# Optimization experiments

Measured on AMD Instinct MI355X. Metric: run time of the kernel, lower is better.

Reference implementation:

```python
import jax, jax.numpy as jnp
import numpy as np

N_GRAPHS = 64

def setup_inputs() -> dict:
    key = jax.random.key(0)
    ks = jax.random.split(key, 8)
    N, E, H = 50000, 600000, 128
    x = jax.random.normal(ks[0], (N, 2), dtype=jnp.float32)
    edge_index = jax.random.randint(ks[1], (2, E), 0, N, dtype=jnp.int64)
    batch = jnp.sort(jax.random.randint(ks[2], (N,), 0, N_GRAPHS, dtype=jnp.int64))
    s = 0.1  # keep tanh out of saturation
    return {
        'x': x,
        'edge_index': edge_index,
        'batch': batch,
        'W1': jax.random.normal(ks[3], (2, H), dtype=jnp.float32) * s,
        'b1': jnp.zeros((H,), jnp.float32),
        'W2': jax.random.normal(ks[4], (H, H), dtype=jnp.float32) * s,
        'b2': jnp.zeros((H,), jnp.float32),
        'W3': jax.random.normal(ks[5], (H, H), dtype=jnp.float32) * s,
        'b3': jnp.zeros((H,), jnp.float32),
        'Wo': jax.random.normal(ks[6], (2 * H, 41), dtype=jnp.float32) * s,
        'bo': jnp.zeros((41,), jnp.float32),
    }

def reference(x, edge_index, batch, W1, b1, W2, b2, W3, b3, Wo, bo):
    N = x.shape[0]
    src, dst = edge_index[0], edge_index[1]
    # GCN symmetric normalization with self loops: deg = in-degree + 1
    ones_e = jnp.ones(src.shape[0], dtype=x.dtype)
    deg = jax.ops.segment_sum(ones_e, dst, num_segments=N) + 1.0
    dinv = jax.lax.rsqrt(deg)                       # [N]
    edge_norm = (dinv[src] * dinv[dst])[:, None]    # [E,1]
    self_norm = (dinv * dinv)[:, None]              # [N,1]

    def gcn(h, W, b):
        h = h @ W                                   # [N,H] transform first
        agg = jax.ops.segment_sum(h[src] * edge_norm, dst, num_segments=N)
        return agg + h * self_norm + b

    h = jnp.tanh(gcn(x, W1, b1))
    h = jnp.tanh(gcn(h, W2, b2))
    h = jnp.tanh(gcn(h, W3, b3))

    # global max pool + global mean pool over graphs
    cnt = jax.ops.segment_sum(jnp.ones(N, dtype=h.dtype), batch, num_segments=N_GRAPHS)
    mx = jax.ops.segment_max(h, batch, num_segments=N_GRAPHS)
    mx = jnp.where(cnt[:, None] > 0, mx, 0.0)
    mean = jax.ops.segment_sum(h, batch, num_segments=N_GRAPHS) / jnp.maximum(cnt, 1.0)[:, None]
    pooled = jnp.concatenate([mx, mean], axis=1)    # [G, 2H]
    return jnp.tanh(pooled @ Wo + bo)               # [G, 41]
```

## Files before the change

### kernel.cpp

```cpp
#include <hip/hip_runtime.h>
#include <math.h>

#define NGRAPH 64
#define SCAN_BLK 1024
#define COLCAP 6144

typedef short short8 __attribute__((ext_vector_type(8)));
typedef float floatx4 __attribute__((ext_vector_type(4)));

__device__ inline unsigned pack_bf16x2(float a, float b) {
    unsigned ua = __float_as_uint(a);
    unsigned ub = __float_as_uint(b);
    ua = (ua + 0x7fffu + ((ua >> 16) & 1u)) >> 16;
    ub = (ub + 0x7fffu + ((ub >> 16) & 1u)) >> 16;
    return ua | (ub << 16);
}
__device__ inline unsigned short bf16_1(float a) {
    unsigned ua = __float_as_uint(a);
    return (unsigned short)((ua + 0x7fffu + ((ua >> 16) & 1u)) >> 16);
}
__device__ inline float bf16lo(unsigned u) { return __uint_as_float(u << 16); }
__device__ inline float bf16hi(unsigned u) { return __uint_as_float(u & 0xffff0000u); }

__device__ inline unsigned fkey(float v) {
    unsigned u = __float_as_uint(v);
    return (v >= 0.f) ? (u | 0x80000000u) : ~u;
}


#define TIDX(u) ((size_t)((qb + (unsigned)(u)) * 4u + (unsigned)q))
#define ACC4() do {                                                       \
    uint4 v0 = t4[TIDX(u0)]; uint4 v1 = t4[TIDX(u1)];                     \
    uint4 v2 = t4[TIDX(u2)]; uint4 v3 = t4[TIDX(u3)];                     \
    a[0] += bf16lo(v0.x); a[1] += bf16hi(v0.x);                           \
    a[2] += bf16lo(v0.y); a[3] += bf16hi(v0.y);                           \
    a[4] += bf16lo(v0.z); a[5] += bf16hi(v0.z);                           \
    a[6] += bf16lo(v0.w); a[7] += bf16hi(v0.w);                           \
    a[0] += bf16lo(v1.x); a[1] += bf16hi(v1.x);                           \
    a[2] += bf16lo(v1.y); a[3] += bf16hi(v1.y);                           \
    a[4] += bf16lo(v1.z); a[5] += bf16hi(v1.z);                           \
    a[6] += bf16lo(v1.w); a[7] += bf16hi(v1.w);                           \
    a[0] += bf16lo(v2.x); a[1] += bf16hi(v2.x);                           \
    a[2] += bf16lo(v2.y); a[3] += bf16hi(v2.y);                           \
    a[4] += bf16lo(v2.z); a[5] += bf16hi(v2.z);                           \
    a[6] += bf16lo(v2.w); a[7] += bf16hi(v2.w);                           \
    a[0] += bf16lo(v3.x); a[1] += bf16hi(v3.x);                           \
    a[2] += bf16lo(v3.y); a[3] += bf16hi(v3.y);                           \
    a[4] += bf16lo(v3.z); a[5] += bf16hi(v3.z);                           \
    a[6] += bf16lo(v3.w); a[7] += bf16hi(v3.w);                           \
} while (0)
#define ACC4M() do {                                                      \
    uint4 v0 = t4[TIDX(u0)]; uint4 v1 = t4[TIDX(u1)];                     \
    uint4 v2 = t4[TIDX(u2)]; uint4 v3 = t4[TIDX(u3)];                     \
    a[0] += bf16lo(v0.x); a[1] += bf16hi(v0.x);                           \
    a[2] += bf16lo(v0.y); a[3] += bf16hi(v0.y);                           \
    a[4] += bf16lo(v0.z); a[5] += bf16hi(v0.z);                           \
    a[6] += bf16lo(v0.w); a[7] += bf16hi(v0.w);                           \
    a[0] = fmaf(m1, bf16lo(v1.x), a[0]); a[1] = fmaf(m1, bf16hi(v1.x), a[1]); \
    a[2] = fmaf(m1, bf16lo(v1.y), a[2]); a[3] = fmaf(m1, bf16hi(v1.y), a[3]); \
    a[4] = fmaf(m1, bf16lo(v1.z), a[4]); a[5] = fmaf(m1, bf16hi(v1.z), a[5]); \
    a[6] = fmaf(m1, bf16lo(v1.w), a[6]); a[7] = fmaf(m1, bf16hi(v1.w), a[7]); \
    a[0] = fmaf(m2, bf16lo(v2.x), a[0]); a[1] = fmaf(m2, bf16hi(v2.x), a[1]); \
    a[2] = fmaf(m2, bf16lo(v2.y), a[2]); a[3] = fmaf(m2, bf16hi(v2.y), a[3]); \
    a[4] = fmaf(m2, bf16lo(v2.z), a[4]); a[5] = fmaf(m2, bf16hi(v2.z), a[5]); \
    a[6] = fmaf(m2, bf16lo(v2.w), a[6]); a[7] = fmaf(m2, bf16hi(v2.w), a[7]); \
    a[0] = fmaf(m3, bf16lo(v3.x), a[0]); a[1] = fmaf(m3, bf16hi(v3.x), a[1]); \
    a[2] = fmaf(m3, bf16lo(v3.y), a[2]); a[3] = fmaf(m3, bf16hi(v3.y), a[3]); \
    a[4] = fmaf(m3, bf16lo(v3.z), a[4]); a[5] = fmaf(m3, bf16hi(v3.z), a[5]); \
    a[6] = fmaf(m3, bf16lo(v3.w), a[6]); a[7] = fmaf(m3, bf16hi(v3.w), a[7]); \
} while (0)


__global__ void pack_count(const int* __restrict__ dst, int E, int* __restrict__ cnt,
                           const float* __restrict__ W2, const float* __restrict__ W3,
                           unsigned* __restrict__ Wt2, unsigned* __restrict__ Wt3) {
    if (blockIdx.x < 32) {
        int b = blockIdx.x;
        const float* W = (b < 16) ? W2 : W3;
        unsigned* Wt = (b < 16) ? Wt2 : Wt3;
        b &= 15;
        int bk = b & 3, bn = b >> 2;
        __shared__ float s[32][33];
        int tx = threadIdx.x & 31, ty = threadIdx.x >> 5;
#pragma unroll
        for (int r = 0; r < 4; ++r)
            s[r * 8 + ty][tx] = W[(bk * 32 + r * 8 + ty) * 128 + bn * 32 + tx];
        __syncthreads();
        int t16 = threadIdx.x & 15, tn = threadIdx.x >> 4;
#pragma unroll
        for (int pass = 0; pass < 2; ++pass) {
            int nl = pass * 16 + tn;
            unsigned pk = pack_bf16x2(s[2 * t16][nl], s[2 * t16 + 1][nl]);
            Wt[(bn * 32 + nl) * 64 + bk * 16 + t16] = pk;
        }
    } else {
        int e = (blockIdx.x - 32) * blockDim.x + threadIdx.x;
        if (e < E) atomicAdd(&cnt[dst[e]], 1);
    }
}


__global__ __launch_bounds__(SCAN_BLK) void scanA(const int* __restrict__ cnt,
                                                  const float* __restrict__ x,
                                                  int* __restrict__ row_ptr,
                                                  int* __restrict__ bsum,
                                                  float* __restrict__ dinv,
                                                  float2* __restrict__ y,
                                                  const int* __restrict__ batch,
                                                  int* __restrict__ ticket,
                                                  int* __restrict__ goff, int N) {
    __shared__ int sm[SCAN_BLK];
    __shared__ int amLast;
    int i = blockIdx.x * SCAN_BLK + threadIdx.x;
    int v = (i < N) ? cnt[i] : 0;
    if (i < N) {
        float dv = rsqrtf((float)v + 1.0f);
        dinv[i] = dv;
        float2 xv = ((const float2*)x)[i];
        y[i] = make_float2(xv.x * dv, xv.y * dv);
    }
    sm[threadIdx.x] = v;
    __syncthreads();
    for (int off = 1; off < SCAN_BLK; off <<= 1) {
        int t = (threadIdx.x >= (unsigned)off) ? sm[threadIdx.x - off] : 0;
        __syncthreads();
        sm[threadIdx.x] += t;
        __syncthreads();
    }
    if (i < N) row_ptr[i] = sm[threadIdx.x] - v;
    if (threadIdx.x == SCAN_BLK - 1) bsum[blockIdx.x] = sm[SCAN_BLK - 1];
    __syncthreads();
    if (threadIdx.x == 0) {
        __threadfence();
        amLast = (atomicAdd(ticket, 1) == (int)gridDim.x - 1);
    }
    __syncthreads();
    if (!amLast) return;
    int nb = (int)gridDim.x;
    int v2 = (threadIdx.x < (unsigned)nb) ? atomicAdd(&bsum[threadIdx.x], 0) : 0;
    sm[threadIdx.x] = v2;
    __syncthreads();
    for (int off = 1; off < SCAN_BLK; off <<= 1) {
        int t = (threadIdx.x >= (unsigned)off) ? sm[threadIdx.x - off] : 0;
        __syncthreads();
        sm[threadIdx.x] += t;
        __syncthreads();
    }
    if (threadIdx.x < (unsigned)nb) bsum[threadIdx.x] = sm[threadIdx.x] - v2;
    if (threadIdx.x <= NGRAPH) {
        int g = threadIdx.x;
        int lo = 0, hi = N;
        while (lo < hi) {
            int mid = (lo + hi) >> 1;
            if (batch[mid] < g) lo = mid + 1; else hi = mid;
        }
        goff[g] = lo;
    }
}

__global__ void fill_kernel(const int* __restrict__ src, const int* __restrict__ dst, int E,
                            const int* __restrict__ row_ptr, const int* __restrict__ bsum,
                            int* __restrict__ cnt, int* __restrict__ col) {
    int e = blockIdx.x * blockDim.x + threadIdx.x;
    if (e < E) {
        int d = dst[e];
        int base = row_ptr[d] + bsum[d >> 10];
        int p = base + atomicSub(&cnt[d], 1) - 1;
        col[p] = src[e];
    }
}


__global__ __launch_bounds__(256) void agg_x_t1(const float2* __restrict__ y,
                                                const int* __restrict__ row_ptr,
                                                const int* __restrict__ bsum,
                                                const int* __restrict__ col,
                                                const float* __restrict__ dinv,
                                                const float* __restrict__ W1,
                                                const float* __restrict__ b1,
                                                unsigned short* __restrict__ h, int N, int E) {
    __shared__ float4 sW[64];
    __shared__ float4 sb[32];
    __shared__ float2 zs[256];
    if (threadIdx.x < 64) sW[threadIdx.x] = ((const float4*)W1)[threadIdx.x];
    if (threadIdx.x < 32) sb[threadIdx.x] = ((const float4*)b1)[threadIdx.x];

    int v = blockIdx.x * 256 + threadIdx.x;
    float2 zv = make_float2(0.f, 0.f);
    if (v < N) {
        int s = row_ptr[v] + bsum[v >> 10];
        int e = (v + 1 < N) ? row_ptr[v + 1] + bsum[(v + 1) >> 10] : E;
        float2 a0 = y[v];
        float2 a1 = make_float2(0.f, 0.f);
        float2 a2 = make_float2(0.f, 0.f);
        float2 a3 = make_float2(0.f, 0.f);
        int j = s;
        for (; j + 4 <= e; j += 4) {
            int u0 = col[j], u1 = col[j + 1], u2 = col[j + 2], u3 = col[j + 3];
            float2 v0 = y[u0], v1 = y[u1], v2 = y[u2], v3 = y[u3];
            a0.x += v0.x; a0.y += v0.y;
            a1.x += v1.x; a1.y += v1.y;
            a2.x += v2.x; a2.y += v2.y;
            a3.x += v3.x; a3.y += v3.y;
        }
        for (; j < e; ++j) {
            float2 vv = y[col[j]];
            a0.x += vv.x; a0.y += vv.y;
        }
        float dv = dinv[v];
        zv = make_float2(dv * (a0.x + a1.x + a2.x + a3.x),
                         dv * (a0.y + a1.y + a2.y + a3.y));
    }
    zs[threadIdx.x] = zv;
    __syncthreads();

    int q = threadIdx.x & 31;
    int rsub = threadIdx.x >> 5;
    float4 w0 = sW[q];
    float4 w1 = sW[32 + q];
    float4 b = sb[q];
    size_t qoff = (size_t)(q >> 3) * N;
#pragma unroll 4
    for (int pass = 0; pass < 32; ++pass) {
        int local = pass * 8 + rsub;
        int row = blockIdx.x * 256 + local;
        if (row >= N) break;
        float2 z = zs[local];
        float ox = tanhf(fmaf(z.x, w0.x, fmaf(z.y, w1.x, b.x)));
        float oy = tanhf(fmaf(z.x, w0.y, fmaf(z.y, w1.y, b.y)));
        float oz = tanhf(fmaf(z.x, w0.z, fmaf(z.y, w1.z, b.z)));
        float ow = tanhf(fmaf(z.x, w0.w, fmaf(z.y, w1.w, b.w)));
        uint2 pk;
        pk.x = pack_bf16x2(ox, oy);
        pk.y = pack_bf16x2(oz, ow);
        ((uint2*)h)[(qoff + row) * 8 + (q & 7)] = pk;
    }
}


__global__ __launch_bounds__(256) void gemm_mfma(const unsigned short* __restrict__ A,
                                                 const unsigned* __restrict__ Wt,
                                                 const float* __restrict__ dinv,
                                                 unsigned short* __restrict__ t, int N) {
    __shared__ unsigned sW[128 * 68];
    const uint4* Wt4 = (const uint4*)Wt;
    for (int i = threadIdx.x; i < 2048; i += 256) {
        int n = i >> 4, c = i & 15;
        *(uint4*)&sW[n * 68 + c * 4] = Wt4[i];
    }
    __syncthreads();
    int l = threadIdx.x & 63;
    int w = threadIdx.x >> 6;
    int lm = l & 15;
    int q4 = l >> 4;

    floatx4 acc[2][8];
#pragma unroll
    for (int i = 0; i < 2; ++i)
#pragma unroll
        for (int j = 0; j < 8; ++j) acc[i][j] = (floatx4){0.f, 0.f, 0.f, 0.f};

    int rowbase = blockIdx.x * 128 + w * 32;
    int k8 = q4 * 8;
#pragma unroll
    for (int ks = 0; ks < 4; ++ks) {
        short8 a[2];
#pragma unroll
        for (int mt = 0; mt < 2; ++mt) {
            int r = min(rowbase + mt * 16 + lm, N - 1);
            a[mt] = *(const short8*)(A + ((size_t)ks * N + r) * 32 + k8);
        }
#pragma unroll
        for (int nt = 0; nt < 8; ++nt) {
            short8 b = *(const short8*)&sW[(nt * 16 + lm) * 68 + ks * 16 + q4 * 4];
#pragma unroll
            for (int mt = 0; mt < 2; ++mt)
                acc[mt][nt] = __builtin_amdgcn_mfma_f32_16x16x32_bf16(b, a[mt], acc[mt][nt], 0, 0, 0);
        }
    }

#pragma unroll
    for (int mt = 0; mt < 2; ++mt) {
        int gr = rowbase + mt * 16 + lm;
        if (gr < N) {
            float dv = dinv[gr];
#pragma unroll
            for (int nt = 0; nt < 8; ++nt) {
                uint2 pk;
                pk.x = pack_bf16x2(acc[mt][nt][0] * dv, acc[mt][nt][1] * dv);
                pk.y = pack_bf16x2(acc[mt][nt][2] * dv, acc[mt][nt][3] * dv);
                *(uint2*)(t + ((size_t)(nt >> 1) * N + gr) * 32 + (nt & 1) * 16 + q4 * 4) = pk;
            }
        }
    }
}


__global__ __launch_bounds__(1024) void agg_kernel(const unsigned short* __restrict__ t,
                                                   const int* __restrict__ row_ptr,
                                                   const int* __restrict__ bsum,
                                                   const int* __restrict__ col,
                                                   const float* __restrict__ dinv,
                                                   const float* __restrict__ bias,
                                                   unsigned short* __restrict__ out, int N, int E) {
    int nchunk = (N + 255) >> 8;
    int bid = (int)blockIdx.x;
    int r8 = bid & 7;
    int qt = r8 >> 1;
    int c = (bid >> 3) * 2 + (r8 & 1);
    if (c >= nchunk) return;

    __shared__ int scol[COLCAP];
    int firstNode = c * 256;
    int lastNode = min(firstNode + 256, N);
    int sBase = row_ptr[firstNode] + bsum[firstNode >> 10];
    int eEnd = (lastNode < N) ? row_ptr[lastNode] + bsum[lastNode >> 10] : E;
    int range = eEnd - sBase;
    bool inLds = (range <= COLCAP);
    if (inLds) {
        for (int i = threadIdx.x; i < range; i += 1024) scol[i] = col[sBase + i];
    }
    __syncthreads();

    int q = threadIdx.x & 3;
    int node = firstNode + ((int)threadIdx.x >> 2);
    if (node >= N) return;
    const uint4* t4 = (const uint4*)t;
    unsigned qb = (unsigned)qt * (unsigned)N;
    int s = row_ptr[node] + bsum[node >> 10];
    int e = (node + 1 < N) ? row_ptr[node + 1] + bsum[(node + 1) >> 10] : E;
    int deg = e - s;

    float a[8];
    {
        uint4 v = t4[TIDX(node)];
        a[0] = bf16lo(v.x); a[1] = bf16hi(v.x);
        a[2] = bf16lo(v.y); a[3] = bf16hi(v.y);
        a[4] = bf16lo(v.z); a[5] = bf16hi(v.z);
        a[6] = bf16lo(v.w); a[7] = bf16hi(v.w);
    }
    int j = 0;
    if (inLds) {
        int sl = s - sBase;
        for (; j + 4 <= deg; j += 4) {
            int u0 = scol[sl + j], u1 = scol[sl + j + 1];
            int u2 = scol[sl + j + 2], u3 = scol[sl + j + 3];
            ACC4();
        }
        if (j < deg) {
            float m1 = (j + 1 < deg) ? 1.f : 0.f;
            float m2 = (j + 2 < deg) ? 1.f : 0.f;
            float m3 = (j + 3 < deg) ? 1.f : 0.f;
            int u0 = scol[sl + j];
            int u1 = scol[sl + min(j + 1, deg - 1)];
            int u2 = scol[sl + min(j + 2, deg - 1)];
            int u3 = scol[sl + min(j + 3, deg - 1)];
            ACC4M();
        }
    } else {
        for (; j + 4 <= deg; j += 4) {
            int u0 = col[s + j], u1 = col[s + j + 1];
            int u2 = col[s + j + 2], u3 = col[s + j + 3];
            ACC4();
        }
        if (j < deg) {
            float m1 = (j + 1 < deg) ? 1.f : 0.f;
            float m2 = (j + 2 < deg) ? 1.f : 0.f;
            float m3 = (j + 3 < deg) ? 1.f : 0.f;
            int u0 = col[s + j];
            int u1 = col[s + min(j + 1, deg - 1)];
            int u2 = col[s + min(j + 2, deg - 1)];
            int u3 = col[s + min(j + 3, deg - 1)];
            ACC4M();
        }
    }

    float dv = dinv[node];
    const float4* b4 = (const float4*)bias;
    float4 b0 = b4[qt * 8 + q * 2];
    float4 b1 = b4[qt * 8 + q * 2 + 1];
    uint4 pk;
    pk.x = pack_bf16x2(tanhf(fmaf(dv, a[0], b0.x)), tanhf(fmaf(dv, a[1], b0.y)));
    pk.y = pack_bf16x2(tanhf(fmaf(dv, a[2], b0.z)), tanhf(fmaf(dv, a[3], b0.w)));
    pk.z = pack_bf16x2(tanhf(fmaf(dv, a[4], b1.x)), tanhf(fmaf(dv, a[5], b1.y)));
    pk.w = pack_bf16x2(tanhf(fmaf(dv, a[6], b1.z)), tanhf(fmaf(dv, a[7], b1.w)));
    ((uint4*)out)[TIDX(node)] = pk;
}


__global__ __launch_bounds__(1024) void agg3_pool(const unsigned short* __restrict__ t,
                                                  const int* __restrict__ row_ptr,
                                                  const int* __restrict__ bsum,
                                                  const int* __restrict__ col,
                                                  const float* __restrict__ dinv,
                                                  const float* __restrict__ bias,
                                                  const int* __restrict__ batch,
                                                  unsigned* __restrict__ pmax,
                                                  float* __restrict__ psum, int N, int E) {
    int nchunk = (N + 255) >> 8;
    int bid = (int)blockIdx.x;
    int r8 = bid & 7;
    int qt = r8 >> 1;
    int c = (bid >> 3) * 2 + (r8 & 1);
    if (c >= nchunk) return;

    __shared__ unsigned smax[2][32];
    __shared__ float ssum[2][32];
    __shared__ int scol[COLCAP];
    if (threadIdx.x < 64) {
        smax[threadIdx.x >> 5][threadIdx.x & 31] = 0u;
        ssum[threadIdx.x >> 5][threadIdx.x & 31] = 0.f;
    }
    int firstNode = c * 256;
    int lastNode = min(firstNode + 256, N);
    int sBase = row_ptr[firstNode] + bsum[firstNode >> 10];
    int eEnd = (lastNode < N) ? row_ptr[lastNode] + bsum[lastNode >> 10] : E;
    int range = eEnd - sBase;
    bool inLds = (range <= COLCAP);
    if (inLds) {
        for (int i = threadIdx.x; i < range; i += 1024) scol[i] = col[sBase + i];
    }
    __syncthreads();

    int q = threadIdx.x & 3;
    int blockBase = firstNode;
    int node = blockBase + ((int)threadIdx.x >> 2);
    bool valid = node < N;
    int nc = valid ? node : N - 1;
    const uint4* t4 = (const uint4*)t;
    unsigned qb = (unsigned)qt * (unsigned)N;
    int s = row_ptr[nc] + bsum[nc >> 10];
    int e = (nc + 1 < N) ? row_ptr[nc + 1] + bsum[(nc + 1) >> 10] : E;
    int deg = valid ? (e - s) : 0;

    float a[8];
    {
        uint4 v = t4[TIDX(nc)];
        a[0] = bf16lo(v.x); a[1] = bf16hi(v.x);
        a[2] = bf16lo(v.y); a[3] = bf16hi(v.y);
        a[4] = bf16lo(v.z); a[5] = bf16hi(v.z);
        a[6] = bf16lo(v.w); a[7] = bf16hi(v.w);
    }
    int j = 0;
    if (inLds) {
        int sl = s - sBase;
        for (; j + 4 <= deg; j += 4) {
            int u0 = scol[sl + j], u1 = scol[sl + j + 1];
            int u2 = scol[sl + j + 2], u3 = scol[sl + j + 3];
            ACC4();
        }
        if (j < deg) {
            float m1 = (j + 1 < deg) ? 1.f : 0.f;
            float m2 = (j + 2 < deg) ? 1.f : 0.f;
            float m3 = (j + 3 < deg) ? 1.f : 0.f;
            int u0 = scol[sl + j];
            int u1 = scol[sl + min(j + 1, deg - 1)];
            int u2 = scol[sl + min(j + 2, deg - 1)];
            int u3 = scol[sl + min(j + 3, deg - 1)];
            ACC4M();
        }
    } else {
        for (; j + 4 <= deg; j += 4) {
            int u0 = col[s + j], u1 = col[s + j + 1];
            int u2 = col[s + j + 2], u3 = col[s + j + 3];
            ACC4();
        }
        if (j < deg) {
            float m1 = (j + 1 < deg) ? 1.f : 0.f;
            float m2 = (j + 2 < deg) ? 1.f : 0.f;
            float m3 = (j + 3 < deg) ? 1.f : 0.f;
            int u0 = col[s + j];
            int u1 = col[s + min(j + 1, deg - 1)];
            int u2 = col[s + min(j + 2, deg - 1)];
            int u3 = col[s + min(j + 3, deg - 1)];
            ACC4M();
        }
    }

    float dv = dinv[nc];
    const float4* b4 = (const float4*)bias;
    float4 b0 = b4[qt * 8 + q * 2];
    float4 b1 = b4[qt * 8 + q * 2 + 1];
    float o[8];
    o[0] = tanhf(fmaf(dv, a[0], b0.x)); o[1] = tanhf(fmaf(dv, a[1], b0.y));
    o[2] = tanhf(fmaf(dv, a[2], b0.z)); o[3] = tanhf(fmaf(dv, a[3], b0.w));
    o[4] = tanhf(fmaf(dv, a[4], b1.x)); o[5] = tanhf(fmaf(dv, a[5], b1.y));
    o[6] = tanhf(fmaf(dv, a[6], b1.z)); o[7] = tanhf(fmaf(dv, a[7], b1.w));

    int g = batch[nc];
    int g0 = batch[min(blockBase, N - 1)];
    int gl = __shfl(g, 0, 64);
    int gh = __shfl(g, 63, 64);

    if (gl == gh) {
        float m[8], sv[8];
#pragma unroll
        for (int k = 0; k < 8; ++k) {
            m[k] = valid ? o[k] : -3.402823466e+38f;
            sv[k] = valid ? o[k] : 0.f;
        }
#pragma unroll
        for (int st = 4; st < 64; st <<= 1) {
#pragma unroll
            for (int k = 0; k < 8; ++k) {
                m[k] = fmaxf(m[k], __shfl_xor(m[k], st, 64));
                sv[k] += __shfl_xor(sv[k], st, 64);
            }
        }
        if (((threadIdx.x & 63) >> 2) == 0) {
            int seg = gl - g0;
            if (seg < 2) {
#pragma unroll
                for (int k = 0; k < 8; ++k) {
                    atomicMax(&smax[seg][q * 8 + k], fkey(m[k]));
                    atomicAdd(&ssum[seg][q * 8 + k], sv[k]);
                }
            } else {
#pragma unroll
                for (int k = 0; k < 8; ++k) {
                    atomicMax(&pmax[gl * 128 + qt * 32 + q * 8 + k], fkey(m[k]));
                    atomicAdd(&psum[gl * 128 + qt * 32 + q * 8 + k], sv[k]);
                }
            }
        }
    } else {
        if (valid) {
            int seg = g - g0;
            if (seg < 2) {
#pragma unroll
                for (int k = 0; k < 8; ++k) {
                    atomicMax(&smax[seg][q * 8 + k], fkey(o[k]));
                    atomicAdd(&ssum[seg][q * 8 + k], o[k]);
                }
            } else {
#pragma unroll
                for (int k = 0; k < 8; ++k) {
                    atomicMax(&pmax[g * 128 + qt * 32 + q * 8 + k], fkey(o[k]));
                    atomicAdd(&psum[g * 128 + qt * 32 + q * 8 + k], o[k]);
                }
            }
        }
    }
    __syncthreads();
    if (threadIdx.x < 64) {
        int seg = threadIdx.x >> 5, cc = threadIdx.x & 31;
        int g0b = batch[min(blockBase, N - 1)];
        int gg = g0b + seg;
        if (gg < NGRAPH) {
            atomicMax(&pmax[gg * 128 + qt * 32 + cc], smax[seg][cc]);
            atomicAdd(&psum[gg * 128 + qt * 32 + cc], ssum[seg][cc]);
        }
    }
}


__global__ __launch_bounds__(128) void pool_final(const unsigned* __restrict__ pmax,
                                                  const float* __restrict__ psum,
                                                  const int* __restrict__ goff,
                                                  const float* __restrict__ Wo,
                                                  const float* __restrict__ bo,
                                                  float* __restrict__ out) {
    __shared__ float p[256];
    int g = blockIdx.x;
    int j = threadIdx.x;
    int cnt = goff[g + 1] - goff[g];
    unsigned key = pmax[g * 128 + j];
    float mx = (key & 0x80000000u) ? __uint_as_float(key ^ 0x80000000u)
                                   : __uint_as_float(~key);
    p[j] = (cnt > 0) ? mx : 0.f;
    p[128 + j] = psum[g * 128 + j] / fmaxf((float)cnt, 1.f);
    __syncthreads();
    if (j < 41) {
        float acc = bo[j];
        for (int k = 0; k < 256; ++k) acc = fmaf(p[k], Wo[k * 41 + j], acc);
        out[g * 41 + j] = tanhf(acc);
    }
}


extern "C" void kernel_launch(void* const* d_in, const int* in_sizes, int n_in,
                              void* d_out, int out_size, void* d_ws, size_t ws_size,
                              hipStream_t stream) {
    const float* x   = (const float*)d_in[0];
    const int*   ei  = (const int*)d_in[1];
    const int* batch = (const int*)d_in[2];
    const float* W1  = (const float*)d_in[3];
    const float* b1  = (const float*)d_in[4];
    const float* W2  = (const float*)d_in[5];
    const float* b2  = (const float*)d_in[6];
    const float* W3  = (const float*)d_in[7];
    const float* b3  = (const float*)d_in[8];
    const float* Wo  = (const float*)d_in[9];
    const float* bo  = (const float*)d_in[10];
    float* outp = (float*)d_out;

    int N = in_sizes[2];
    int E = in_sizes[1] / 2;
    const int* src = ei;
    const int* dst = ei + E;

    char* p = (char*)d_ws;
    auto alloc = [&](size_t bytes) -> char* {
        char* q = p;
        p += (bytes + 255) & ~(size_t)255;
        return q;
    };
    unsigned short* t   = (unsigned short*)alloc((size_t)N * 128 * 2);
    unsigned short* hb  = (unsigned short*)alloc((size_t)N * 128 * 2);
    float* dinv   = (float*)alloc((size_t)N * 4);
    int*   rowp   = (int*)alloc((size_t)(N + 1) * 4);
    int*   col    = (int*)alloc((size_t)E * 4);
    int*   goff   = (int*)alloc(65 * 4);
    float2* y     = (float2*)alloc((size_t)N * 8);
    unsigned* Wt2 = (unsigned*)alloc(128 * 64 * 4);
    unsigned* Wt3 = (unsigned*)alloc(128 * 64 * 4);
    int nscan = (N + SCAN_BLK - 1) / SCAN_BLK;
    int*   bsum   = (int*)alloc((size_t)nscan * 4);
    size_t cntB = ((size_t)N * 4 + 255) & ~(size_t)255;
    char* zbase = alloc(cntB + 256 + NGRAPH * 128 * 4 * 2);
    int*      cnt  = (int*)zbase;
    int*      tick = (int*)(zbase + cntB);
    unsigned* pmax = (unsigned*)(zbase + cntB + 256);
    float*    psum = (float*)(zbase + cntB + 256 + NGRAPH * 128 * 4);

    (void)hipMemsetAsync(zbase, 0, cntB + 256 + NGRAPH * 128 * 4 * 2, stream);

    pack_count<<<32 + (E + 255) / 256, 256, 0, stream>>>(dst, E, cnt, W2, W3, Wt2, Wt3);
    scanA<<<nscan, SCAN_BLK, 0, stream>>>(cnt, x, rowp, bsum, dinv, y, batch, tick, goff, N);
    fill_kernel<<<(E + 255) / 256, 256, 0, stream>>>(src, dst, E, rowp, bsum, cnt, col);

    int nchunk = (N + 255) >> 8;
    int nchunkR = (nchunk + 1) & ~1;
    int nblk = nchunkR * 4;

    agg_x_t1<<<(N + 255) / 256, 256, 0, stream>>>(y, rowp, bsum, col, dinv, W1, b1, hb, N, E);
    gemm_mfma<<<(N + 127) / 128, 256, 0, stream>>>(hb, Wt2, dinv, t, N);
    agg_kernel<<<nblk, 1024, 0, stream>>>(t, rowp, bsum, col, dinv, b2, hb, N, E);
    gemm_mfma<<<(N + 127) / 128, 256, 0, stream>>>(hb, Wt3, dinv, t, N);
    agg3_pool<<<nblk, 1024, 0, stream>>>(t, rowp, bsum, col, dinv, b3, batch, pmax, psum, N, E);

    pool_final<<<NGRAPH, 128, 0, stream>>>(pmax, psum, goff, Wo, bo, outp);
}
```

Before: 255.9 us.

## Record edge ranks during counting and split layer-1 aggregation across 4 lanes per node

The counting kernel now saves each edge's atomicAdd return value as its rank, so the CSR fill kernel computes positions directly and no longer needs a second round of atomics on the counters. The first-layer aggregation uses 64 nodes per block with 4 lanes per node instead of one thread per node. The block's column indices are staged in LDS when they fit, and the partial sums are combined with wave shuffles. This is meant to cut fill atomic contention and improve load balance and memory parallelism in the gather, at the cost of an extra E-sized rank buffer and four times as many blocks for the small transform step.

```diff
diff --git a/kernel.cpp b/kernel.cpp
--- a/kernel.cpp
+++ b/kernel.cpp
@@ -4,6 +4,7 @@
 #define NGRAPH 64
 #define SCAN_BLK 1024
 #define COLCAP 6144
+#define AXCAP 2560
 
 typedef short short8 __attribute__((ext_vector_type(8)));
 typedef float floatx4 __attribute__((ext_vector_type(4)));
@@ -72,6 +73,7 @@
 
 
 __global__ void pack_count(const int* __restrict__ dst, int E, int* __restrict__ cnt,
+                           int* __restrict__ rank,
                            const float* __restrict__ W2, const float* __restrict__ W3,
                            unsigned* __restrict__ Wt2, unsigned* __restrict__ Wt3) {
     if (blockIdx.x < 32) {
@@ -95,7 +97,7 @@
         }
     } else {
         int e = (blockIdx.x - 32) * blockDim.x + threadIdx.x;
-        if (e < E) atomicAdd(&cnt[dst[e]], 1);
+        if (e < E) rank[e] = atomicAdd(&cnt[dst[e]], 1);
     }
 }
 
@@ -160,12 +162,11 @@
 
 __global__ void fill_kernel(const int* __restrict__ src, const int* __restrict__ dst, int E,
                             const int* __restrict__ row_ptr, const int* __restrict__ bsum,
-                            int* __restrict__ cnt, int* __restrict__ col) {
+                            const int* __restrict__ rank, int* __restrict__ col) {
     int e = blockIdx.x * blockDim.x + threadIdx.x;
     if (e < E) {
         int d = dst[e];
-        int base = row_ptr[d] + bsum[d >> 10];
-        int p = base + atomicSub(&cnt[d], 1) - 1;
+        int p = row_ptr[d] + bsum[d >> 10] + rank[e];
         col[p] = src[e];
     }
 }
@@ -181,37 +182,58 @@
                                                 unsigned short* __restrict__ h, int N, int E) {
     __shared__ float4 sW[64];
     __shared__ float4 sb[32];
-    __shared__ float2 zs[256];
+    __shared__ float2 zs[64];
+    __shared__ int scol[AXCAP];
     if (threadIdx.x < 64) sW[threadIdx.x] = ((const float4*)W1)[threadIdx.x];
-    if (threadIdx.x < 32) sb[threadIdx.x] = ((const float4*)b1)[threadIdx.x];
-
-    int v = blockIdx.x * 256 + threadIdx.x;
-    float2 zv = make_float2(0.f, 0.f);
-    if (v < N) {
-        int s = row_ptr[v] + bsum[v >> 10];
-        int e = (v + 1 < N) ? row_ptr[v + 1] + bsum[(v + 1) >> 10] : E;
-        float2 a0 = y[v];
-        float2 a1 = make_float2(0.f, 0.f);
-        float2 a2 = make_float2(0.f, 0.f);
-        float2 a3 = make_float2(0.f, 0.f);
-        int j = s;
-        for (; j + 4 <= e; j += 4) {
-            int u0 = col[j], u1 = col[j + 1], u2 = col[j + 2], u3 = col[j + 3];
-            float2 v0 = y[u0], v1 = y[u1], v2 = y[u2], v3 = y[u3];
-            a0.x += v0.x; a0.y += v0.y;
-            a1.x += v1.x; a1.y += v1.y;
-            a2.x += v2.x; a2.y += v2.y;
-            a3.x += v3.x; a3.y += v3.y;
-        }
-        for (; j < e; ++j) {
-            float2 vv = y[col[j]];
-            a0.x += vv.x; a0.y += vv.y;
-        }
-        float dv = dinv[v];
-        zv = make_float2(dv * (a0.x + a1.x + a2.x + a3.x),
-                         dv * (a0.y + a1.y + a2.y + a3.y));
-    }
-    zs[threadIdx.x] = zv;
+    if (threadIdx.x >= 64 && threadIdx.x < 96) sb[threadIdx.x - 64] = ((const float4*)b1)[threadIdx.x - 64];
+
+    int firstNode = blockIdx.x * 64;
+    int lastNode = min(firstNode + 64, N);
+    int sBase = row_ptr[firstNode] + bsum[firstNode >> 10];
+    int eEnd = (lastNode < N) ? row_ptr[lastNode] + bsum[lastNode >> 10] : E;
+    int range = eEnd - sBase;
+    bool inLds = (range <= AXCAP);
+    if (inLds) {
+        for (int i = threadIdx.x; i < range; i += 256) scol[i] = col[sBase + i];
+    }
+    __syncthreads();
+
+    int grp = threadIdx.x >> 2;
+    int l4 = threadIdx.x & 3;
+    int node = firstNode + grp;
+    float ax = 0.f, ay = 0.f;
+    if (node < N) {
+        int s = row_ptr[node] + bsum[node >> 10];
+        int e = (node + 1 < N) ? row_ptr[node + 1] + bsum[(node + 1) >> 10] : E;
+        int deg = e - s;
+        if (inLds) {
+            int sl = s - sBase;
+            int j = l4;
+            for (; j + 4 < deg; j += 8) {
+                float2 v0 = y[scol[sl + j]];
+                float2 v1 = y[scol[sl + j + 4]];
+                ax += v0.x; ay += v0.y;
+                ax += v1.x; ay += v1.y;
+            }
+            if (j < deg) { float2 v = y[scol[sl + j]]; ax += v.x; ay += v.y; }
+        } else {
+            int j = l4;
+            for (; j + 4 < deg; j += 8) {
+                float2 v0 = y[col[s + j]];
+                float2 v1 = y[col[s + j + 4]];
+                ax += v0.x; ay += v0.y;
+                ax += v1.x; ay += v1.y;
+            }
+            if (j < deg) { float2 v = y[col[s + j]]; ax += v.x; ay += v.y; }
+        }
+    }
+    ax += __shfl_xor(ax, 1, 64); ay += __shfl_xor(ay, 1, 64);
+    ax += __shfl_xor(ax, 2, 64); ay += __shfl_xor(ay, 2, 64);
+    if (l4 == 0 && node < N) {
+        float2 self = y[node];
+        float dv = dinv[node];
+        zs[grp] = make_float2(dv * (ax + self.x), dv * (ay + self.y));
+    }
     __syncthreads();
 
     int q = threadIdx.x & 31;
@@ -220,10 +242,10 @@
     float4 w1 = sW[32 + q];
     float4 b = sb[q];
     size_t qoff = (size_t)(q >> 3) * N;
-#pragma unroll 4
-    for (int pass = 0; pass < 32; ++pass) {
+#pragma unroll
+    for (int pass = 0; pass < 8; ++pass) {
         int local = pass * 8 + rsub;
-        int row = blockIdx.x * 256 + local;
+        int row = firstNode + local;
         if (row >= N) break;
         float2 z = zs[local];
         float ox = tanhf(fmaf(z.x, w0.x, fmaf(z.y, w1.x, b.x)));
@@ -610,6 +632,7 @@
     float* dinv   = (float*)alloc((size_t)N * 4);
     int*   rowp   = (int*)alloc((size_t)(N + 1) * 4);
     int*   col    = (int*)alloc((size_t)E * 4);
+    int*   rank   = (int*)alloc((size_t)E * 4);
     int*   goff   = (int*)alloc(65 * 4);
     float2* y     = (float2*)alloc((size_t)N * 8);
     unsigned* Wt2 = (unsigned*)alloc(128 * 64 * 4);
@@ -625,15 +648,15 @@
 
     (void)hipMemsetAsync(zbase, 0, cntB + 256 + NGRAPH * 128 * 4 * 2, stream);
 
-    pack_count<<<32 + (E + 255) / 256, 256, 0, stream>>>(dst, E, cnt, W2, W3, Wt2, Wt3);
+    pack_count<<<32 + (E + 255) / 256, 256, 0, stream>>>(dst, E, cnt, rank, W2, W3, Wt2, Wt3);
     scanA<<<nscan, SCAN_BLK, 0, stream>>>(cnt, x, rowp, bsum, dinv, y, batch, tick, goff, N);
-    fill_kernel<<<(E + 255) / 256, 256, 0, stream>>>(src, dst, E, rowp, bsum, cnt, col);
+    fill_kernel<<<(E + 255) / 256, 256, 0, stream>>>(src, dst, E, rowp, bsum, rank, col);
 
     int nchunk = (N + 255) >> 8;
     int nchunkR = (nchunk + 1) & ~1;
     int nblk = nchunkR * 4;
 
-    agg_x_t1<<<(N + 255) / 256, 256, 0, stream>>>(y, rowp, bsum, col, dinv, W1, b1, hb, N, E);
+    agg_x_t1<<<(N + 63) / 64, 256, 0, stream>>>(y, rowp, bsum, col, dinv, W1, b1, hb, N, E);
     gemm_mfma<<<(N + 127) / 128, 256, 0, stream>>>(hb, Wt2, dinv, t, N);
     agg_kernel<<<nblk, 1024, 0, stream>>>(t, rowp, bsum, col, dinv, b2, hb, N, E);
     gemm_mfma<<<(N + 127) / 128, 256, 0, stream>>>(hb, Wt3, dinv, t, N);
```

Measured after the change: 228.7 us. 10.6% less time.
